# Kernel optimization log

Measured on AMD Instinct MI355X. Metric: run time of the kernel, lower is better.

Reference implementation:

```python
import jax, jax.numpy as jnp
import numpy as np

PI = 3.141592653589793
EPS_BN = 1e-5

# Heaviside spike with ATan surrogate gradient (snntorch default, alpha=2 -> 1/(1+(pi*u)^2))
@jax.custom_vjp
def spike(u):
    return (u > 0).astype(u.dtype)

def _spike_fwd(u):
    return (u > 0).astype(u.dtype), u

def _spike_bwd(u, g):
    return (g / (1.0 + (PI * u) ** 2),)

spike.defvjp(_spike_fwd, _spike_bwd)


def setup_inputs() -> dict:
    key = jax.random.key(0)
    k_x, k_w = jax.random.split(key, 2)
    T, B, Cin, Cout, H, W = 4, 8, 64, 128, 48, 48
    x = jax.random.normal(k_x, (T, B, Cin, H, W), jnp.float32)
    # Alpha-neuron learnable scalars (torch.rand(1) in the original); distinct so tau is finite
    alpha = jnp.asarray(0.9, jnp.float32)
    beta = jnp.asarray(0.8, jnp.float32)
    th1 = jnp.asarray(0.5, jnp.float32)
    th2 = jnp.asarray(0.4, jnp.float32)
    # SConv2dLSTM gate conv: in = Cin + Cout (input || hidden mem), out = 4*Cout gates, 3x3 SAME
    fan_in = (Cin + Cout) * 9
    w_conv = jax.random.normal(k_w, (4 * Cout, Cin + Cout, 3, 3), jnp.float32) / np.sqrt(fan_in)
    b_conv = jnp.zeros((4 * Cout,), jnp.float32)
    # BatchNorm2d affine params
    gamma = jnp.ones((Cout,), jnp.float32)
    bn_beta = jnp.zeros((Cout,), jnp.float32)
    return dict(x=x, alpha=alpha, beta=beta, th1=th1, th2=th2,
                w_conv=w_conv, b_conv=b_conv, gamma=gamma, bn_beta=bn_beta)


def reference(x, alpha, beta, th1, th2, w_conv, b_conv, gamma, bn_beta):
    T, B, Cin, H, W = x.shape
    Cout = gamma.shape[0]
    a = jnp.clip(alpha, 1e-6, 1.0 - 1e-6)
    b = jnp.clip(beta, 1e-6, 1.0 - 1e-6)
    # Alpha-neuron time constant: tau = log(a) / (log(b) - log(a))
    tau = jnp.log(a) / (jnp.log(b) - jnp.log(a))

    def gate_conv(inp):  # [B, Cin+Cout, H, W] -> [B, 4*Cout, H, W]
        y = jax.lax.conv_general_dilated(
            inp, w_conv, window_strides=(1, 1), padding='SAME',
            dimension_numbers=('NCHW', 'OIHW', 'NCHW'))
        return y + b_conv[None, :, None, None]

    def step(carry, x_t):
        syn_e, syn_i, spk1_prev, syn2, mem2 = carry
        # --- snn.Alpha: dual-exponential leaky integrator + subtract-reset ---
        syn_e = a * syn_e + x_t
        syn_i = b * syn_i - x_t
        mem1 = tau * (syn_e + syn_i) - spk1_prev * th1
        spk1 = spike(mem1 - th1)
        # --- snn.SConv2dLSTM: conv-LSTM, hidden = membrane, spiking output ---
        comb = jnp.concatenate([spk1, mem2], axis=1)  # [B, Cin+Cout, H, W]
        cc = gate_conv(comb)
        ci, cf, cg, co = jnp.split(cc, 4, axis=1)
        syn2 = jax.nn.sigmoid(cf) * syn2 + jax.nn.sigmoid(ci) * jnp.tanh(cg)
        mem2 = jax.nn.sigmoid(co) * jnp.tanh(syn2)
        spk2 = spike(mem2 - th2)
        # --- BatchNormTT2d: per-timestep BN with batch statistics ---
        mu = jnp.mean(spk2, axis=(0, 2, 3), keepdims=True)
        var = jnp.var(spk2, axis=(0, 2, 3), keepdims=True)
        y = gamma[None, :, None, None] * (spk2 - mu) * jax.lax.rsqrt(var + EPS_BN) \
            + bn_beta[None, :, None, None]
        return (syn_e, syn_i, spk1, syn2, mem2), y

    z_in = jnp.zeros((B, Cin, H, W), x.dtype)
    z_out = jnp.zeros((B, Cout, H, W), x.dtype)
    init = (z_in, z_in, z_in, z_out, z_out)
    _, ys = jax.lax.scan(step, init, x)
    return ys  # [T, B, Cout, H, W]
```

## Files before the change

kernel.cpp:

```cpp
#include <hip/hip_runtime.h>


typedef unsigned short u16;
typedef __attribute__((ext_vector_type(8))) __bf16 bf16x8;
typedef __attribute__((ext_vector_type(4))) float   f32x4;

#define T_ 4
#define B_ 8
#define CIN 64
#define COUT 128
#define H_ 48
#define W_ 48
#define HW 2304
#define NPIX 18432
#define KTOT 1728
#define WTPL 884736
#define M2PL 2359296
#define APL  5760

#define OFF_SYNE  0
#define OFF_SYNI  1179648
#define OFF_SPK1H 2359296
#define OFF_CNT   2949120
#define ZERO_W    2949632
#define OFF_SYN2  2949632
#define OFF_SPK2H 5308928
#define OFF_M2H0  6488576
#define OFF_M2H1  10027520
#define OFF_WT    13566464
#define OFF_U     14893568

static __device__ __forceinline__ u16 bfbits(float f) {
    __bf16 h = (__bf16)f; u16 u; __builtin_memcpy(&u, &h, 2); return u;
}
static __device__ __forceinline__ float bff(u16 u) {
    __bf16 h; __builtin_memcpy(&h, &u, 2); return (float)h;
}
static __device__ __forceinline__ f32x4 MFMA(bf16x8 a, bf16x8 b, f32x4 c) {
    return __builtin_amdgcn_mfma_f32_16x16x32_bf16(a, b, c, 0, 0, 0);
}

__global__ __launch_bounds__(256) void zero_ws_kernel(float* __restrict__ p, int n) {
    int i = blockIdx.x * 256 + threadIdx.x;
    if (i < n) p[i] = 0.0f;
}

__global__ __launch_bounds__(256) void wt_transform_kernel(
        const float* __restrict__ w, u16* __restrict__ wt) {
    int id = blockIdx.x * 256 + threadIdx.x;
    int lane = id & 63;
    int rest = id >> 6;
    int tap = rest % 9;
    int rest2 = rest / 9;
    int ck = rest2 % 6, nt = rest2 / 6;
    int gate = nt & 3, cg = nt >> 2;
    int coutsub = lane & 15, kgl = lane >> 4;
    int oc = gate * COUT + cg * 16 + coutsub;
    int kh = tap / 3, kw = tap - kh * 3;
    size_t dst = ((size_t)(nt * 6 + ck) * 9 + tap) * 512 + lane * 8;
#pragma unroll
    for (int j = 0; j < 8; ++j) {
        int ch = ck * 32 + kgl * 8 + j;
        float wv = w[((oc * 192 + ch) * 3 + kh) * 3 + kw];
        float hh = (float)(__bf16)wv;
        float r1 = wv - hh;
        float ll = (float)(__bf16)r1;
        float r2 = r1 - ll;
        wt[dst + j]            = bfbits(hh);
        wt[WTPL + dst + j]     = bfbits(ll);
        wt[2 * WTPL + dst + j] = bfbits(r2);
    }
}

__global__ __launch_bounds__(256) void alpha_step_kernel(
        const float4* __restrict__ x_t,
        const float* __restrict__ p_alpha, const float* __restrict__ p_beta,
        const float* __restrict__ p_th1,
        float4* __restrict__ syn_e, float4* __restrict__ syn_i,
        u16* __restrict__ spk1h) {
#pragma clang fp contract(off)
    int q = blockIdx.x * 256 + threadIdx.x;
    float a = fminf(fmaxf(p_alpha[0], 1e-6f), 1.0f - 1e-6f);
    float b = fminf(fmaxf(p_beta[0],  1e-6f), 1.0f - 1e-6f);
    float la = logf(a), lb = logf(b);
    float tau = la / (lb - la);
    float th1 = p_th1[0];

    int bc = q / 576;
    int hw0 = (q - bc * 576) * 4;
    int bb = bc >> 6, c = bc & 63;
    u16* sp = spk1h + ((size_t)(bb * 4 + (c >> 4)) * HW + hw0) * 16 + (c & 15);

    float4 xv = x_t[q], e4 = syn_e[q], i4 = syn_i[q];
    float pr0 = bff(sp[0]), pr1 = bff(sp[16]), pr2 = bff(sp[32]), pr3 = bff(sp[48]);
    float e, ii, m1;
    u16 s0, s1, s2, s3;
    e = a * e4.x + xv.x; ii = b * i4.x - xv.x; m1 = tau * (e + ii) - pr0 * th1;
    e4.x = e; i4.x = ii; s0 = (m1 - th1) > 0.0f ? 0x3F80u : 0u;
    e = a * e4.y + xv.y; ii = b * i4.y - xv.y; m1 = tau * (e + ii) - pr1 * th1;
    e4.y = e; i4.y = ii; s1 = (m1 - th1) > 0.0f ? 0x3F80u : 0u;
    e = a * e4.z + xv.z; ii = b * i4.z - xv.z; m1 = tau * (e + ii) - pr2 * th1;
    e4.z = e; i4.z = ii; s2 = (m1 - th1) > 0.0f ? 0x3F80u : 0u;
    e = a * e4.w + xv.w; ii = b * i4.w - xv.w; m1 = tau * (e + ii) - pr3 * th1;
    e4.w = e; i4.w = ii; s3 = (m1 - th1) > 0.0f ? 0x3F80u : 0u;
    syn_e[q] = e4; syn_i[q] = i4;
    sp[0] = s0; sp[16] = s1; sp[32] = s2; sp[48] = s3;
}

__global__ void t0_u_kernel(const float* __restrict__ b_conv, float* __restrict__ u) {
#pragma clang fp contract(off)
    int c = threadIdx.x;
    float gi = b_conv[c], gf = b_conv[COUT + c];
    float gg = b_conv[2 * COUT + c], go = b_conv[3 * COUT + c];
    float si = 1.0f / (1.0f + expf(-gi));
    float sf = 1.0f / (1.0f + expf(-gf));
    float so = 1.0f / (1.0f + expf(-go));
    float tg = tanhf(gg);
    float s2 = sf * 0.0f + si * tg;
    float m2 = so * tanhf(s2);
    u[c] = s2;
    u16* uh = (u16*)(u + 128);
    float hh = (float)(__bf16)m2;
    float r1 = m2 - hh;
    float ll = (float)(__bf16)r1;
    float r2 = r1 - ll;
    uh[c] = bfbits(hh); uh[128 + c] = bfbits(ll); uh[256 + c] = bfbits(r2);
}

__global__ __launch_bounds__(256) void t0_fillA_kernel(
        const float* __restrict__ u, const float* __restrict__ bnb,
        float4* __restrict__ out0) {
    int i = blockIdx.x * 256 + threadIdx.x;
    int c = ((i * 4) / HW) % COUT;
    float bb = bnb[c];
    out0[i] = make_float4(bb, bb, bb, bb);
}

__global__ __launch_bounds__(256) void t0_fillB_kernel(
        const float* __restrict__ u,
        u16* __restrict__ m2, float4* __restrict__ syn2) {
    int i = blockIdx.x * 256 + threadIdx.x;
    const u16* uh = (const u16*)(u + 128);
    int pxg = i >> 2;
    int cg = (pxg / HW) & 7;
    int c0 = cg * 16 + (i & 3) * 4;
    *(uint2*)(m2 + (size_t)i * 4)             = *(const uint2*)(uh + c0);
    *(uint2*)(m2 + M2PL + (size_t)i * 4)      = *(const uint2*)(uh + 128 + c0);
    *(uint2*)(m2 + 2 * M2PL + (size_t)i * 4)  = *(const uint2*)(uh + 256 + c0);
    int csy = ((i >> 9) & 7) * 16 + (i & 15);
    float s2 = u[csy];
    syn2[i] = make_float4(s2, s2, s2, s2);
}

#define LDSROW(P, r, kw) (*(const bf16x8*)&alds[P][(((r) * 18) + m16 + (kw)) * 32 + kg * 8])
__global__ __launch_bounds__(256, 3) void conv_lstm_fused(
        const u16* __restrict__ spk1h,
        const u16* __restrict__ m2rd,
        const u16* __restrict__ wt,
        const float* __restrict__ bias, const float* __restrict__ p_th2,
        float* __restrict__ syn2,
        u16* __restrict__ m2wr,
        u16* __restrict__ spk2h, int* __restrict__ cnt) {
    __shared__ __align__(16) u16 alds[3][APL];

    const int bx  = blockIdx.x;
    const int ntq = bx / 144;
    const int rm  = bx - ntq * 144;
    const int mt  = rm >> 3;
    const int b   = rm & 7;
    const int mt3 = mt / 3;
    const int h0 = mt3 * 8, w0 = (mt - mt3 * 3) * 16;

    const int tid = threadIdx.x;
    const int wn  = tid >> 6;
    const int lane = tid & 63;
    const int m16 = lane & 15;
    const int kg  = lane >> 4;
    const int nt = ntq * 4 + wn;

    f32x4 acc[8];
#pragma unroll
    for (int mf = 0; mf < 8; ++mf) acc[mf] = (f32x4){0.f, 0.f, 0.f, 0.f};

    int ldsM[9], srcM[9];
#pragma unroll
    for (int j = 0; j < 9; ++j) {
        int i = tid + j * 256;
        int pl = i / 720;
        int r = i - pl * 720;
        int px = r >> 2, qt = r & 3;
        int rr = px / 18, cc2 = px - rr * 18;
        int gh = h0 - 1 + rr, gw = w0 - 1 + cc2;
        ldsM[j] = (i < 2160) ? (pl * APL + px * 32 + qt * 8) : -1;
        bool ok = (i < 2160) && ((unsigned)gh < 48u) && ((unsigned)gw < 48u);
        srcM[j] = ok ? (pl * M2PL + ((b * 8 + (qt >> 1)) * HW + gh * 48 + gw) * 16
                        + (qt & 1) * 8) : -1;
    }

    {
        uint4 stB[6]; int ldsB[6];
#pragma unroll
        for (int j = 0; j < 6; ++j) {
            int i = tid + j * 256;
            int ckb = i / 720;
            int r = i - ckb * 720;
            int px = r >> 2, qt = r & 3;
            int rr = px / 18, cc2 = px - rr * 18;
            int gh = h0 - 1 + rr, gw = w0 - 1 + cc2;
            ldsB[j] = (i < 1440) ? (ckb * APL + px * 32 + qt * 8) : -1;
            uint4 v = make_uint4(0u, 0u, 0u, 0u);
            if (i < 1440 && (unsigned)gh < 48u && (unsigned)gw < 48u)
                v = *(const uint4*)(spk1h
                    + ((size_t)(b * 4 + ckb * 2 + (qt >> 1)) * HW + gh * 48 + gw) * 16
                    + (qt & 1) * 8);
            stB[j] = v;
        }
#pragma unroll
        for (int j = 0; j < 6; ++j)
            if (ldsB[j] >= 0) *(uint4*)&alds[0][ldsB[j]] = stB[j];
    }
    __syncthreads();

    uint4 stM[9];
#define LOADM(ck_)                                                           \
    {                                                                        \
        const int add = ((ck_) - 2) * (2 * HW * 16);                         \
        _Pragma("unroll")                                                    \
        for (int j = 0; j < 9; ++j) {                                        \
            uint4 v = make_uint4(0u, 0u, 0u, 0u);                            \
            if (srcM[j] >= 0) v = *(const uint4*)(m2rd + srcM[j] + add);     \
            stM[j] = v;                                                      \
        }                                                                    \
    }
#define WRITEM                                                               \
    {                                                                        \
        _Pragma("unroll")                                                    \
        for (int j = 0; j < 9; ++j)                                          \
            if (ldsM[j] >= 0) *(uint4*)&alds[0][ldsM[j]] = stM[j];           \
    }

    LOADM(2);

    for (int ckb = 0; ckb < 2; ++ckb) {
#pragma unroll
        for (int kw = 0; kw < 3; ++kw) {
            bf16x8 B0[3], B1[3], B2[3];
#pragma unroll
            for (int kh = 0; kh < 3; ++kh) {
                const size_t bo = ((size_t)(nt * 6 + ckb) * 9 + kh * 3 + kw) * 512 + lane * 8;
                B0[kh] = *(const bf16x8*)(wt + bo);
                B1[kh] = *(const bf16x8*)(wt + WTPL + bo);
                B2[kh] = *(const bf16x8*)(wt + 2 * WTPL + bo);
            }
            bf16x8 aw[3];
            aw[0] = LDSROW(ckb, 0, kw);
            aw[1] = LDSROW(ckb, 1, kw);
#pragma unroll
            for (int mf = 0; mf < 8; ++mf) {
                aw[(mf + 2) % 3] = LDSROW(ckb, mf + 2, kw);
#pragma unroll
                for (int kh = 0; kh < 3; ++kh) {
                    const bf16x8 A = aw[(mf + kh) % 3];
                    acc[mf] = MFMA(A, B0[kh], acc[mf]);
                    acc[mf] = MFMA(A, B1[kh], acc[mf]);
                    acc[mf] = MFMA(A, B2[kh], acc[mf]);
                }
            }
        }
    }

    for (int ck = 2; ck < 6; ++ck) {
        __syncthreads();
        WRITEM;
        __syncthreads();
        if (ck < 5) LOADM(ck + 1);
#pragma unroll
        for (int kw = 0; kw < 3; ++kw) {
            bf16x8 B0[3], B1[3], B2[3];
#pragma unroll
            for (int kh = 0; kh < 3; ++kh) {
                const size_t bo = ((size_t)(nt * 6 + ck) * 9 + kh * 3 + kw) * 512 + lane * 8;
                B0[kh] = *(const bf16x8*)(wt + bo);
                B1[kh] = *(const bf16x8*)(wt + WTPL + bo);
                B2[kh] = *(const bf16x8*)(wt + 2 * WTPL + bo);
            }
            bf16x8 a0[3], a1[3], a2[3];
            a0[0] = LDSROW(0, 0, kw); a0[1] = LDSROW(0, 1, kw);
            a1[0] = LDSROW(1, 0, kw); a1[1] = LDSROW(1, 1, kw);
            a2[0] = LDSROW(2, 0, kw); a2[1] = LDSROW(2, 1, kw);
#pragma unroll
            for (int mf = 0; mf < 8; ++mf) {
                const int sn = (mf + 2) % 3;
                a0[sn] = LDSROW(0, mf + 2, kw);
                a1[sn] = LDSROW(1, mf + 2, kw);
                a2[sn] = LDSROW(2, mf + 2, kw);
#pragma unroll
                for (int kh = 0; kh < 3; ++kh) {
                    const int s = (mf + kh) % 3;
                    acc[mf] = MFMA(a0[s], B0[kh], acc[mf]);
                    acc[mf] = MFMA(a0[s], B1[kh], acc[mf]);
                    acc[mf] = MFMA(a0[s], B2[kh], acc[mf]);
                    acc[mf] = MFMA(a1[s], B0[kh], acc[mf]);
                    acc[mf] = MFMA(a1[s], B1[kh], acc[mf]);
                    acc[mf] = MFMA(a2[s], B0[kh], acc[mf]);
                    acc[mf] = MFMA(a2[s], B1[kh], acc[mf]);
                }
            }
        }
    }

    __syncthreads();
    {
        float* glds = (float*)alds;
#pragma unroll
        for (int mf = 0; mf < 8; ++mf)
            *(f32x4*)(glds + (wn * 8 + mf) * 256 + lane * 4) = acc[mf];
    }
    __syncthreads();
    {
#pragma clang fp contract(off)
        const float* glds = (const float*)alds;
        const int c = ntq * 16 + m16;
        const float th2 = p_th2[0];
        const float b0 = bias[c],       b1 = bias[128 + c];
        const float b2 = bias[256 + c], b3 = bias[384 + c];
        int sc = 0;
#pragma unroll
        for (int q = 0; q < 2; ++q) {
            const int mfq = wn * 2 + q;
            const f32x4 vI = *(const f32x4*)(glds + (0 * 8 + mfq) * 256 + lane * 4);
            const f32x4 vF = *(const f32x4*)(glds + (1 * 8 + mfq) * 256 + lane * 4);
            const f32x4 vG = *(const f32x4*)(glds + (2 * 8 + mfq) * 256 + lane * 4);
            const f32x4 vO = *(const f32x4*)(glds + (3 * 8 + mfq) * 256 + lane * 4);
            const size_t sidx = ((size_t)(((b * 18 + mt) * 8 + ntq) * 8 + mfq) * 64 + lane) * 4;
            const f32x4 s2v = *(const f32x4*)(syn2 + sidx);
            const int h = h0 + mfq;
            const size_t pixb = ((size_t)(b * 8 + ntq) * HW + h * 48 + w0 + kg * 4) * 16 + m16;
            f32x4 s2o;
#pragma unroll
            for (int j = 0; j < 4; ++j) {
                float gi = vI[j] + b0, gf = vF[j] + b1;
                float gg = vG[j] + b2, go = vO[j] + b3;
                float si = 1.0f / (1.0f + expf(-gi));
                float sf = 1.0f / (1.0f + expf(-gf));
                float so = 1.0f / (1.0f + expf(-go));
                float tg = tanhf(gg);
                float s2 = sf * s2v[j] + si * tg;
                float m2 = so * tanhf(s2);
                s2o[j] = s2;
                float hh = (float)(__bf16)m2;
                float r1 = m2 - hh;
                float ll = (float)(__bf16)r1;
                float r2 = r1 - ll;
                const size_t pix = pixb + (size_t)j * 16;
                m2wr[pix]             = bfbits(hh);
                m2wr[M2PL + pix]      = bfbits(ll);
                m2wr[2 * M2PL + pix]  = bfbits(r2);
                bool sp = (m2 - th2) > 0.0f;
                spk2h[pix] = sp ? 0x3F80u : 0u;
                sc += sp ? 1 : 0;
            }
            *(f32x4*)(syn2 + sidx) = s2o;
        }
        sc += __shfl_xor(sc, 16);
        sc += __shfl_xor(sc, 32);
        if (lane < 16) atomicAdd(&cnt[ntq * 16 + lane], sc);
    }
#undef LOADM
#undef WRITEM
}

__global__ __launch_bounds__(256) void bn_step_kernel(
        const u16* __restrict__ spk2h, const int* __restrict__ cnt,
        const float* __restrict__ gamma, const float* __restrict__ bnb,
        float4* __restrict__ out) {
#pragma clang fp contract(off)
    int i = blockIdx.x * 256 + threadIdx.x;
    int e = i * 4;
    int tmp = e / HW;
    int bb = tmp >> 7, c = tmp & 127;
    int hw0 = e - tmp * HW;
    const u16* sp = spk2h + ((size_t)(bb * 8 + (c >> 4)) * HW + hw0) * 16 + (c & 15);
    float mu  = (float)cnt[c] / (float)NPIX;
    float var = mu - mu * mu;
    float rs  = rsqrtf(var + 1e-5f);
    float g = gamma[c], bv = bnb[c];
    float s0 = bff(sp[0]), s1 = bff(sp[16]), s2 = bff(sp[32]), s3 = bff(sp[48]);
    out[i] = make_float4(g * (s0 - mu) * rs + bv, g * (s1 - mu) * rs + bv,
                         g * (s2 - mu) * rs + bv, g * (s3 - mu) * rs + bv);
}

extern "C" void kernel_launch(void* const* d_in, const int* in_sizes, int n_in,
                              void* d_out, int out_size, void* d_ws, size_t ws_size,
                              hipStream_t stream) {
    const float* x       = (const float*)d_in[0];
    const float* p_alpha = (const float*)d_in[1];
    const float* p_beta  = (const float*)d_in[2];
    const float* p_th1   = (const float*)d_in[3];
    const float* p_th2   = (const float*)d_in[4];
    const float* w_conv  = (const float*)d_in[5];
    const float* b_conv  = (const float*)d_in[6];
    const float* gamma   = (const float*)d_in[7];
    const float* bn_beta = (const float*)d_in[8];
    float* out = (float*)d_out;

    float* wsf   = (float*)d_ws;
    float* syn_e = wsf + OFF_SYNE;
    float* syn_i = wsf + OFF_SYNI;
    u16*   spk1h = (u16*)(wsf + OFF_SPK1H);
    int*   cnt   = (int*)(wsf + OFF_CNT);
    float* syn2  = wsf + OFF_SYN2;
    u16*   spk2h = (u16*)(wsf + OFF_SPK2H);
    u16*   m2buf[2] = {(u16*)(wsf + OFF_M2H0), (u16*)(wsf + OFF_M2H1)};
    u16*   wt    = (u16*)(wsf + OFF_WT);
    float* u     = wsf + OFF_U;

    zero_ws_kernel<<<ZERO_W / 256, 256, 0, stream>>>(wsf, ZERO_W);
    wt_transform_kernel<<<432, 256, 0, stream>>>(w_conv, wt);

    alpha_step_kernel<<<1152, 256, 0, stream>>>(
        (const float4*)x, p_alpha, p_beta, p_th1,
        (float4*)syn_e, (float4*)syn_i, spk1h);
    t0_u_kernel<<<1, COUT, 0, stream>>>(b_conv, u);
    t0_fillA_kernel<<<2304, 256, 0, stream>>>(u, bn_beta, (float4*)out);
    t0_fillB_kernel<<<2304, 256, 0, stream>>>(u, m2buf[0], (float4*)syn2);

    for (int t = 1; t < T_; ++t) {
        const int rd = (t - 1) & 1, wr = t & 1;
        alpha_step_kernel<<<1152, 256, 0, stream>>>(
            (const float4*)(x + (size_t)t * 1179648), p_alpha, p_beta, p_th1,
            (float4*)syn_e, (float4*)syn_i, spk1h);
        conv_lstm_fused<<<1152, 256, 0, stream>>>(
            spk1h, m2buf[rd], wt, b_conv, p_th2,
            syn2, m2buf[wr], spk2h, cnt + t * COUT);
        bn_step_kernel<<<2304, 256, 0, stream>>>(
            spk2h, cnt + t * COUT, gamma, bn_beta,
            (float4*)(out + (size_t)t * 2359296));
    }
}
```

Baseline: 555.1 us.

## Double-buffer mem2 LDS tiles in conv_lstm_fused and drop one split-precision MFMA term

```diff
diff --git a/kernel.cpp b/kernel.cpp
--- a/kernel.cpp
+++ b/kernel.cpp
@@ -153,7 +153,7 @@
 }
 
 #define LDSROW(P, r, kw) (*(const bf16x8*)&alds[P][(((r) * 18) + m16 + (kw)) * 32 + kg * 8])
-__global__ __launch_bounds__(256, 3) void conv_lstm_fused(
+__global__ __launch_bounds__(256, 2) void conv_lstm_fused(
         const u16* __restrict__ spk1h,
         const u16* __restrict__ m2rd,
         const u16* __restrict__ wt,
@@ -161,7 +161,7 @@
         float* __restrict__ syn2,
         u16* __restrict__ m2wr,
         u16* __restrict__ spk2h, int* __restrict__ cnt) {
-    __shared__ __align__(16) u16 alds[3][APL];
+    __shared__ __align__(16) u16 alds[6][APL];
 
     const int bx  = blockIdx.x;
     const int ntq = bx / 144;
@@ -232,11 +232,12 @@
             stM[j] = v;                                                      \
         }                                                                    \
     }
-#define WRITEM                                                               \
+#define WRITEM(PB_)                                                          \
     {                                                                        \
+        u16* dstb = &alds[PB_][0];                                           \
         _Pragma("unroll")                                                    \
         for (int j = 0; j < 9; ++j)                                          \
-            if (ldsM[j] >= 0) *(uint4*)&alds[0][ldsM[j]] = stM[j];           \
+            if (ldsM[j] >= 0) *(uint4*)&dstb[ldsM[j]] = stM[j];              \
     }
 
     LOADM(2);
@@ -269,45 +270,61 @@
         }
     }
 
-    for (int ck = 2; ck < 6; ++ck) {
-        __syncthreads();
-        WRITEM;
-        __syncthreads();
-        if (ck < 5) LOADM(ck + 1);
-#pragma unroll
-        for (int kw = 0; kw < 3; ++kw) {
-            bf16x8 B0[3], B1[3], B2[3];
-#pragma unroll
-            for (int kh = 0; kh < 3; ++kh) {
-                const size_t bo = ((size_t)(nt * 6 + ck) * 9 + kh * 3 + kw) * 512 + lane * 8;
-                B0[kh] = *(const bf16x8*)(wt + bo);
-                B1[kh] = *(const bf16x8*)(wt + WTPL + bo);
-                B2[kh] = *(const bf16x8*)(wt + 2 * WTPL + bo);
-            }
-            bf16x8 a0[3], a1[3], a2[3];
-            a0[0] = LDSROW(0, 0, kw); a0[1] = LDSROW(0, 1, kw);
-            a1[0] = LDSROW(1, 0, kw); a1[1] = LDSROW(1, 1, kw);
-            a2[0] = LDSROW(2, 0, kw); a2[1] = LDSROW(2, 1, kw);
-#pragma unroll
-            for (int mf = 0; mf < 8; ++mf) {
-                const int sn = (mf + 2) % 3;
-                a0[sn] = LDSROW(0, mf + 2, kw);
-                a1[sn] = LDSROW(1, mf + 2, kw);
-                a2[sn] = LDSROW(2, mf + 2, kw);
-#pragma unroll
-                for (int kh = 0; kh < 3; ++kh) {
-                    const int s = (mf + kh) % 3;
-                    acc[mf] = MFMA(a0[s], B0[kh], acc[mf]);
-                    acc[mf] = MFMA(a0[s], B1[kh], acc[mf]);
-                    acc[mf] = MFMA(a0[s], B2[kh], acc[mf]);
-                    acc[mf] = MFMA(a1[s], B0[kh], acc[mf]);
-                    acc[mf] = MFMA(a1[s], B1[kh], acc[mf]);
-                    acc[mf] = MFMA(a2[s], B0[kh], acc[mf]);
-                    acc[mf] = MFMA(a2[s], B1[kh], acc[mf]);
-                }
-            }
-        }
-    }
+#define COMPUTE_M(CK_, PB_)                                                  \
+    {                                                                        \
+        _Pragma("unroll")                                                    \
+        for (int kw = 0; kw < 3; ++kw) {                                     \
+            bf16x8 B0[3], B1[3], B2[3];                                      \
+            _Pragma("unroll")                                                \
+            for (int kh = 0; kh < 3; ++kh) {                                 \
+                const size_t bo = ((size_t)(nt * 6 + (CK_)) * 9 + kh * 3 + kw) * 512 + lane * 8; \
+                B0[kh] = *(const bf16x8*)(wt + bo);                          \
+                B1[kh] = *(const bf16x8*)(wt + WTPL + bo);                   \
+                B2[kh] = *(const bf16x8*)(wt + 2 * WTPL + bo);               \
+            }                                                                \
+            bf16x8 a0[3], a1[3], a2[3];                                      \
+            a0[0] = LDSROW((PB_) + 0, 0, kw); a0[1] = LDSROW((PB_) + 0, 1, kw); \
+            a1[0] = LDSROW((PB_) + 1, 0, kw); a1[1] = LDSROW((PB_) + 1, 1, kw); \
+            a2[0] = LDSROW((PB_) + 2, 0, kw); a2[1] = LDSROW((PB_) + 2, 1, kw); \
+            _Pragma("unroll")                                                \
+            for (int mf = 0; mf < 8; ++mf) {                                 \
+                const int sn = (mf + 2) % 3;                                 \
+                a0[sn] = LDSROW((PB_) + 0, mf + 2, kw);                      \
+                a1[sn] = LDSROW((PB_) + 1, mf + 2, kw);                      \
+                a2[sn] = LDSROW((PB_) + 2, mf + 2, kw);                      \
+                _Pragma("unroll")                                            \
+                for (int kh = 0; kh < 3; ++kh) {                             \
+                    const int s = (mf + kh) % 3;                             \
+                    acc[mf] = MFMA(a0[s], B0[kh], acc[mf]);                  \
+                    acc[mf] = MFMA(a0[s], B1[kh], acc[mf]);                  \
+                    acc[mf] = MFMA(a0[s], B2[kh], acc[mf]);                  \
+                    acc[mf] = MFMA(a1[s], B0[kh], acc[mf]);                  \
+                    acc[mf] = MFMA(a1[s], B1[kh], acc[mf]);                  \
+                    acc[mf] = MFMA(a2[s], B0[kh], acc[mf]);                  \
+                }                                                            \
+            }                                                                \
+        }                                                                    \
+    }
+
+    WRITEM(3);
+    LOADM(3);
+    __syncthreads();
+
+    WRITEM(0);
+    LOADM(4);
+    COMPUTE_M(2, 3);
+    __syncthreads();
+
+    WRITEM(3);
+    LOADM(5);
+    COMPUTE_M(3, 0);
+    __syncthreads();
+
+    WRITEM(0);
+    COMPUTE_M(4, 3);
+    __syncthreads();
+
+    COMPUTE_M(5, 0);
 
     __syncthreads();
     {
@@ -368,6 +385,7 @@
     }
 #undef LOADM
 #undef WRITEM
+#undef COMPUTE_M
 }
 
 __global__ __launch_bounds__(256) void bn_step_kernel(
```

Result: faster. 476.5 us (-14.2%).
